# Performance work log

Hardware: AMD Instinct MI355X
Metric: run time of the kernel (lower is better)

## Reference

```python
import jax, jax.numpy as jnp
import numpy as np

HIDDEN = 2048
VOCAB = 50257


def setup_inputs() -> dict:
    key = jax.random.key(0)
    ks = jax.random.split(key, 9)
    s = 1.0 / np.sqrt(HIDDEN)
    return {
        "input": jax.random.randint(ks[0], (1,), 0, VOCAB, dtype=jnp.int64) if jax.config.jax_enable_x64 else jax.random.randint(ks[0], (1,), 0, VOCAB, dtype=jnp.int32),
        "hidden": jax.random.normal(ks[1], (1, 1, HIDDEN), dtype=jnp.float32),
        "embedding": jax.random.normal(ks[2], (VOCAB, HIDDEN), dtype=jnp.float32),
        "w_ih": jax.random.uniform(ks[3], (3 * HIDDEN, HIDDEN), jnp.float32, -s, s),
        "w_hh": jax.random.uniform(ks[4], (3 * HIDDEN, HIDDEN), jnp.float32, -s, s),
        "b_ih": jax.random.uniform(ks[5], (3 * HIDDEN,), jnp.float32, -s, s),
        "b_hh": jax.random.uniform(ks[6], (3 * HIDDEN,), jnp.float32, -s, s),
        "out_w": jax.random.uniform(ks[7], (VOCAB, HIDDEN), jnp.float32, -s, s),
        "out_b": jax.random.uniform(ks[8], (VOCAB,), jnp.float32, -s, s),
    }


def reference(input, hidden, embedding, w_ih, w_hh, b_ih, b_hh, out_w, out_b):
    # embedding lookup + view(1,1,-1) + relu  -> x: [H]
    x = jax.nn.relu(embedding[input[0]])
    h = hidden[0, 0]  # [H]
    # PyTorch GRU single step: gates ordered (r, z, n)
    gi = w_ih @ x + b_ih  # [3H]
    gh = w_hh @ h + b_hh  # [3H]
    i_r, i_z, i_n = jnp.split(gi, 3)
    h_r, h_z, h_n = jnp.split(gh, 3)
    r = jax.nn.sigmoid(i_r + h_r)
    z = jax.nn.sigmoid(i_z + h_z)
    n = jnp.tanh(i_n + r * h_n)
    h_new = (1.0 - z) * n + z * h  # [H]
    # output projection (nn.Linear: x @ W.T + b) + log_softmax(dim=1)
    logits = out_w @ h_new + out_b  # [V]
    logp = jax.nn.log_softmax(logits)[None, :]  # [1, V]
    return logp, h_new[None, None, :]
```

## Files before the change

kernel.cpp:

```cpp
#include <hip/hip_runtime.h>
#include <math.h>

#define H 2048
#define V 50257

__device__ __forceinline__ float wave_reduce_sum(float v) {
#pragma unroll
    for (int off = 32; off > 0; off >>= 1)
        v += __shfl_down(v, off, 64);
    return v;
}

__device__ __forceinline__ float wave_reduce_max(float v) {
#pragma unroll
    for (int off = 32; off > 0; off >>= 1)
        v = fmaxf(v, __shfl_down(v, off, 64));
    return v;
}

__global__ void k_embed(const int* __restrict__ idx_p,
                        const float* __restrict__ emb,
                        float* __restrict__ x) {
    int i = blockIdx.x * blockDim.x + threadIdx.x;
    if (i < H) {
        long idx = (long)idx_p[0];
        float v = emb[idx * (long)H + i];
        x[i] = v > 0.f ? v : 0.f;
    }
}

__global__ __launch_bounds__(384) void k_gru(
    const float* __restrict__ w_ih, const float* __restrict__ w_hh,
    const float* __restrict__ b_ih, const float* __restrict__ b_hh,
    const float* __restrict__ x, const float* __restrict__ hid,
    float* __restrict__ hnew_ws, float* __restrict__ hnew_out) {
    __shared__ float xs[H];
    __shared__ float hs[H];
    __shared__ float partial[6];
    int tid = threadIdx.x;
    for (int i = tid; i < H / 4; i += 384) {
        ((float4*)xs)[i] = ((const float4*)x)[i];
        ((float4*)hs)[i] = ((const float4*)hid)[i];
    }
    __syncthreads();

    int wid = tid >> 6, lane = tid & 63;
    int j = blockIdx.x;
    int gate = wid % 3;
    const float* W = (wid < 3) ? w_ih : w_hh;
    const float* vec = (wid < 3) ? xs : hs;
    const float* row = W + (size_t)(gate * H + j) * (size_t)H;

    float acc = 0.f;
#pragma unroll
    for (int it = 0; it < 8; ++it) {
        float4 w4 = ((const float4*)row)[it * 64 + lane];
        float4 v4 = ((const float4*)vec)[it * 64 + lane];
        acc += w4.x * v4.x + w4.y * v4.y + w4.z * v4.z + w4.w * v4.w;
    }
    acc = wave_reduce_sum(acc);
    if (lane == 0) partial[wid] = acc;
    __syncthreads();

    if (tid == 0) {
        float i_r = partial[0] + b_ih[j];
        float i_z = partial[1] + b_ih[H + j];
        float i_n = partial[2] + b_ih[2 * H + j];
        float h_r = partial[3] + b_hh[j];
        float h_z = partial[4] + b_hh[H + j];
        float h_n = partial[5] + b_hh[2 * H + j];
        float r = 1.f / (1.f + expf(-(i_r + h_r)));
        float z = 1.f / (1.f + expf(-(i_z + h_z)));
        float n = tanhf(i_n + r * h_n);
        float hv = (1.f - z) * n + z * hs[j];
        hnew_ws[j] = hv;
        hnew_out[j] = hv;
    }
}

__global__ __launch_bounds__(256) void k_logits(
    const float* __restrict__ out_w, const float* __restrict__ out_b,
    const float* __restrict__ hnew, float* __restrict__ logits) {
    __shared__ float hs[H];
    int tid = threadIdx.x;
    for (int i = tid; i < H / 4; i += 256)
        ((float4*)hs)[i] = ((const float4*)hnew)[i];
    __syncthreads();

    int wid = tid >> 6, lane = tid & 63;
    int r = blockIdx.x * 4 + wid;
    if (r >= V) return;
    const float* row = out_w + (size_t)r * (size_t)H;

    float acc = 0.f;
#pragma unroll
    for (int it = 0; it < 8; ++it) {
        float4 w4 = ((const float4*)row)[it * 64 + lane];
        float4 v4 = ((const float4*)hs)[it * 64 + lane];
        acc += w4.x * v4.x + w4.y * v4.y + w4.z * v4.z + w4.w * v4.w;
    }
    acc = wave_reduce_sum(acc);
    if (lane == 0) logits[r] = acc + out_b[r];
}

__global__ __launch_bounds__(1024) void k_lse(const float* __restrict__ logits,
                                              float* __restrict__ stats) {
    __shared__ float red[16];
    __shared__ float m_s;
    int tid = threadIdx.x;

    float m = -INFINITY;
    for (int i = tid; i < V; i += 1024) m = fmaxf(m, logits[i]);
    m = wave_reduce_max(m);
    if ((tid & 63) == 0) red[tid >> 6] = m;
    __syncthreads();
    if (tid < 16) {
        m = red[tid];
#pragma unroll
        for (int off = 8; off > 0; off >>= 1)
            m = fmaxf(m, __shfl_down(m, off, 64));
        if (tid == 0) m_s = m;
    }
    __syncthreads();
    float gm = m_s;

    float s = 0.f;
    for (int i = tid; i < V; i += 1024) s += expf(logits[i] - gm);
    s = wave_reduce_sum(s);
    __syncthreads();
    if ((tid & 63) == 0) red[tid >> 6] = s;
    __syncthreads();
    if (tid == 0) {
        float tot = 0.f;
#pragma unroll
        for (int w = 0; w < 16; ++w) tot += red[w];
        stats[0] = gm;
        stats[1] = logf(tot);
    }
}

__global__ void k_finalize(const float* __restrict__ logits,
                           const float* __restrict__ stats,
                           float* __restrict__ out) {
    int i = blockIdx.x * blockDim.x + threadIdx.x;
    if (i < V) out[i] = logits[i] - stats[0] - stats[1];
}

extern "C" void kernel_launch(void* const* d_in, const int* in_sizes, int n_in,
                              void* d_out, int out_size, void* d_ws, size_t ws_size,
                              hipStream_t stream) {
    const int*   idx    = (const int*)d_in[0];
    const float* hidden = (const float*)d_in[1];
    const float* emb    = (const float*)d_in[2];
    const float* w_ih   = (const float*)d_in[3];
    const float* w_hh   = (const float*)d_in[4];
    const float* b_ih   = (const float*)d_in[5];
    const float* b_hh   = (const float*)d_in[6];
    const float* out_w  = (const float*)d_in[7];
    const float* out_b  = (const float*)d_in[8];

    float* out = (float*)d_out;
    float* ws  = (float*)d_ws;
    float* x      = ws;
    float* hnew   = ws + H;
    float* logits = ws + 2 * H;
    float* stats  = ws + 2 * H + ((V + 63) & ~63);

    k_embed<<<(H + 255) / 256, 256, 0, stream>>>(idx, emb, x);
    k_gru<<<H, 384, 0, stream>>>(w_ih, w_hh, b_ih, b_hh, x, hidden, hnew, out + V);
    k_logits<<<(V + 3) / 4, 256, 0, stream>>>(out_w, out_b, hnew, logits);
    k_lse<<<1, 1024, 0, stream>>>(logits, stats);
    k_finalize<<<(V + 255) / 256, 256, 0, stream>>>(logits, stats, out);
}
```

Measured before the change: 117.8 us.

## Fuse embed into GRU, compute online softmax stats in logits kernel

```diff
diff --git a/kernel.cpp b/kernel.cpp
--- a/kernel.cpp
+++ b/kernel.cpp
@@ -3,6 +3,10 @@
 
 #define H 2048
 #define V 50257
+
+#define LOGITS_BLOCKS 2048
+#define LOGITS_WAVES (LOGITS_BLOCKS * 4)
+#define FIN_BLOCKS 52
 
 __device__ __forceinline__ float wave_reduce_sum(float v) {
 #pragma unroll
@@ -11,64 +15,64 @@
     return v;
 }
 
-__device__ __forceinline__ float wave_reduce_max(float v) {
-#pragma unroll
-    for (int off = 32; off > 0; off >>= 1)
-        v = fmaxf(v, __shfl_down(v, off, 64));
-    return v;
-}
-
-__global__ void k_embed(const int* __restrict__ idx_p,
-                        const float* __restrict__ emb,
-                        float* __restrict__ x) {
-    int i = blockIdx.x * blockDim.x + threadIdx.x;
-    if (i < H) {
-        long idx = (long)idx_p[0];
-        float v = emb[idx * (long)H + i];
-        x[i] = v > 0.f ? v : 0.f;
-    }
-}
-
 __global__ __launch_bounds__(384) void k_gru(
+    const int* __restrict__ idx_p,
+    const float* __restrict__ emb,
+    const float* __restrict__ hid,
     const float* __restrict__ w_ih, const float* __restrict__ w_hh,
     const float* __restrict__ b_ih, const float* __restrict__ b_hh,
-    const float* __restrict__ x, const float* __restrict__ hid,
     float* __restrict__ hnew_ws, float* __restrict__ hnew_out) {
     __shared__ float xs[H];
     __shared__ float hs[H];
-    __shared__ float partial[6];
+    __shared__ float partial[6][2];
     int tid = threadIdx.x;
+
+    long idx = (long)idx_p[0];
+    const float4* embrow = (const float4*)(emb + idx * (long)H);
     for (int i = tid; i < H / 4; i += 384) {
-        ((float4*)xs)[i] = ((const float4*)x)[i];
+        float4 e = embrow[i];
+        e.x = fmaxf(e.x, 0.f); e.y = fmaxf(e.y, 0.f);
+        e.z = fmaxf(e.z, 0.f); e.w = fmaxf(e.w, 0.f);
+        ((float4*)xs)[i] = e;
         ((float4*)hs)[i] = ((const float4*)hid)[i];
     }
     __syncthreads();
 
     int wid = tid >> 6, lane = tid & 63;
-    int j = blockIdx.x;
     int gate = wid % 3;
-    const float* W = (wid < 3) ? w_ih : w_hh;
+    const float* W   = (wid < 3) ? w_ih : w_hh;
     const float* vec = (wid < 3) ? xs : hs;
-    const float* row = W + (size_t)(gate * H + j) * (size_t)H;
+    int j0 = blockIdx.x;
+    int j1 = blockIdx.x + 1024;
+    const float4* r0 = (const float4*)(W + ((size_t)gate * H + j0) * (size_t)H);
+    const float4* r1 = (const float4*)(W + ((size_t)gate * H + j1) * (size_t)H);
 
-    float acc = 0.f;
+    float4 vreg[8];
+#pragma unroll
+    for (int it = 0; it < 8; ++it)
+        vreg[it] = ((const float4*)vec)[it * 64 + lane];
+
+    float a0 = 0.f, a1 = 0.f;
 #pragma unroll
     for (int it = 0; it < 8; ++it) {
-        float4 w4 = ((const float4*)row)[it * 64 + lane];
-        float4 v4 = ((const float4*)vec)[it * 64 + lane];
-        acc += w4.x * v4.x + w4.y * v4.y + w4.z * v4.z + w4.w * v4.w;
+        float4 wa = r0[it * 64 + lane];
+        float4 wb = r1[it * 64 + lane];
+        a0 += wa.x * vreg[it].x + wa.y * vreg[it].y + wa.z * vreg[it].z + wa.w * vreg[it].w;
+        a1 += wb.x * vreg[it].x + wb.y * vreg[it].y + wb.z * vreg[it].z + wb.w * vreg[it].w;
     }
-    acc = wave_reduce_sum(acc);
-    if (lane == 0) partial[wid] = acc;
+    a0 = wave_reduce_sum(a0);
+    a1 = wave_reduce_sum(a1);
+    if (lane == 0) { partial[wid][0] = a0; partial[wid][1] = a1; }
     __syncthreads();
 
-    if (tid == 0) {
-        float i_r = partial[0] + b_ih[j];
-        float i_z = partial[1] + b_ih[H + j];
-        float i_n = partial[2] + b_ih[2 * H + j];
-        float h_r = partial[3] + b_hh[j];
-        float h_z = partial[4] + b_hh[H + j];
-        float h_n = partial[5] + b_hh[2 * H + j];
+    if (tid < 2) {
+        int j = (tid == 0) ? j0 : j1;
+        float i_r = partial[0][tid] + b_ih[j];
+        float i_z = partial[1][tid] + b_ih[H + j];
+        float i_n = partial[2][tid] + b_ih[2 * H + j];
+        float h_r = partial[3][tid] + b_hh[j];
+        float h_z = partial[4][tid] + b_hh[H + j];
+        float h_n = partial[5][tid] + b_hh[2 * H + j];
         float r = 1.f / (1.f + expf(-(i_r + h_r)));
         float z = 1.f / (1.f + expf(-(i_z + h_z)));
         float n = tanhf(i_n + r * h_n);
@@ -80,70 +84,93 @@
 
 __global__ __launch_bounds__(256) void k_logits(
     const float* __restrict__ out_w, const float* __restrict__ out_b,
-    const float* __restrict__ hnew, float* __restrict__ logits) {
+    const float* __restrict__ hnew,
+    float* __restrict__ logits, float2* __restrict__ partials) {
     __shared__ float hs[H];
+    __shared__ float pm[4], ps[4];
     int tid = threadIdx.x;
     for (int i = tid; i < H / 4; i += 256)
         ((float4*)hs)[i] = ((const float4*)hnew)[i];
     __syncthreads();
 
     int wid = tid >> 6, lane = tid & 63;
-    int r = blockIdx.x * 4 + wid;
-    if (r >= V) return;
-    const float* row = out_w + (size_t)r * (size_t)H;
+    float4 vreg[8];
+#pragma unroll
+    for (int it = 0; it < 8; ++it)
+        vreg[it] = ((const float4*)hs)[it * 64 + lane];
 
-    float acc = 0.f;
+    float m = -INFINITY, s = 0.f;
+    for (int r = blockIdx.x * 4 + wid; r < V; r += LOGITS_WAVES) {
+        const float4* row = (const float4*)(out_w + (size_t)r * (size_t)H);
+        float acc = 0.f;
 #pragma unroll
-    for (int it = 0; it < 8; ++it) {
-        float4 w4 = ((const float4*)row)[it * 64 + lane];
-        float4 v4 = ((const float4*)hs)[it * 64 + lane];
-        acc += w4.x * v4.x + w4.y * v4.y + w4.z * v4.z + w4.w * v4.w;
+        for (int it = 0; it < 8; ++it) {
+            float4 w4 = row[it * 64 + lane];
+            acc += w4.x * vreg[it].x + w4.y * vreg[it].y + w4.z * vreg[it].z + w4.w * vreg[it].w;
+        }
+        acc = wave_reduce_sum(acc);
+        if (lane == 0) {
+            float l = acc + out_b[r];
+            logits[r] = l;
+            float M = fmaxf(m, l);
+            s = s * __expf(m - M) + __expf(l - M);
+            m = M;
+        }
     }
-    acc = wave_reduce_sum(acc);
-    if (lane == 0) logits[r] = acc + out_b[r];
-}
-
-__global__ __launch_bounds__(1024) void k_lse(const float* __restrict__ logits,
-                                              float* __restrict__ stats) {
-    __shared__ float red[16];
-    __shared__ float m_s;
-    int tid = threadIdx.x;
-
-    float m = -INFINITY;
-    for (int i = tid; i < V; i += 1024) m = fmaxf(m, logits[i]);
-    m = wave_reduce_max(m);
-    if ((tid & 63) == 0) red[tid >> 6] = m;
-    __syncthreads();
-    if (tid < 16) {
-        m = red[tid];
-#pragma unroll
-        for (int off = 8; off > 0; off >>= 1)
-            m = fmaxf(m, __shfl_down(m, off, 64));
-        if (tid == 0) m_s = m;
-    }
-    __syncthreads();
-    float gm = m_s;
-
-    float s = 0.f;
-    for (int i = tid; i < V; i += 1024) s += expf(logits[i] - gm);
-    s = wave_reduce_sum(s);
-    __syncthreads();
-    if ((tid & 63) == 0) red[tid >> 6] = s;
+    if (lane == 0) { pm[wid] = m; ps[wid] = s; }
     __syncthreads();
     if (tid == 0) {
-        float tot = 0.f;
-#pragma unroll
-        for (int w = 0; w < 16; ++w) tot += red[w];
-        stats[0] = gm;
-        stats[1] = logf(tot);
+        float M = fmaxf(fmaxf(pm[0], pm[1]), fmaxf(pm[2], pm[3]));
+        float S = ps[0] * __expf(pm[0] - M) + ps[1] * __expf(pm[1] - M) +
+                  ps[2] * __expf(pm[2] - M) + ps[3] * __expf(pm[3] - M);
+        partials[blockIdx.x] = make_float2(M, S);
     }
 }
 
-__global__ void k_finalize(const float* __restrict__ logits,
-                           const float* __restrict__ stats,
-                           float* __restrict__ out) {
-    int i = blockIdx.x * blockDim.x + threadIdx.x;
-    if (i < V) out[i] = logits[i] - stats[0] - stats[1];
+__global__ __launch_bounds__(256) void k_finalize(
+    const float* __restrict__ logits, const float2* __restrict__ partials,
+    float* __restrict__ out) {
+    __shared__ float pm[4], ps[4];
+    __shared__ float cs;
+    int tid = threadIdx.x;
+
+    float m = -INFINITY, s = 0.f;
+    for (int i = tid; i < LOGITS_BLOCKS; i += 256) {
+        float2 p = partials[i];
+        float M = fmaxf(m, p.x);
+        s = s * __expf(m - M) + p.y * __expf(p.x - M);
+        m = M;
+    }
+#pragma unroll
+    for (int off = 32; off > 0; off >>= 1) {
+        float om = __shfl_down(m, off, 64);
+        float os = __shfl_down(s, off, 64);
+        float M = fmaxf(m, om);
+        s = s * __expf(m - M) + os * __expf(om - M);
+        m = M;
+    }
+    int wid = tid >> 6, lane = tid & 63;
+    if (lane == 0) { pm[wid] = m; ps[wid] = s; }
+    __syncthreads();
+    if (tid == 0) {
+        float M = fmaxf(fmaxf(pm[0], pm[1]), fmaxf(pm[2], pm[3]));
+        float S = ps[0] * __expf(pm[0] - M) + ps[1] * __expf(pm[1] - M) +
+                  ps[2] * __expf(pm[2] - M) + ps[3] * __expf(pm[3] - M);
+        cs = M + logf(S);
+    }
+    __syncthreads();
+    float C = cs;
+
+    int gid = blockIdx.x * 256 + tid;
+    const int nf = V / 4;
+    for (int i = gid; i < nf; i += FIN_BLOCKS * 256) {
+        float4 l4 = ((const float4*)logits)[i];
+        l4.x -= C; l4.y -= C; l4.z -= C; l4.w -= C;
+        ((float4*)out)[i] = l4;
+    }
+    if (gid == 0) {
+        for (int i = nf * 4; i < V; ++i) out[i] = logits[i] - C;
+    }
 }
 
 extern "C" void kernel_launch(void* const* d_in, const int* in_sizes, int n_in,
@@ -161,14 +188,12 @@
 
     float* out = (float*)d_out;
     float* ws  = (float*)d_ws;
-    float* x      = ws;
-    float* hnew   = ws + H;
-    float* logits = ws + 2 * H;
-    float* stats  = ws + 2 * H + ((V + 63) & ~63);
+    float*  hnew     = ws;
+    float*  logits   = ws + H;
+    float2* partials = (float2*)(ws + H + ((V + 1) & ~1));
 
-    k_embed<<<(H + 255) / 256, 256, 0, stream>>>(idx, emb, x);
-    k_gru<<<H, 384, 0, stream>>>(w_ih, w_hh, b_ih, b_hh, x, hidden, hnew, out + V);
-    k_logits<<<(V + 3) / 4, 256, 0, stream>>>(out_w, out_b, hnew, logits);
-    k_lse<<<1, 1024, 0, stream>>>(logits, stats);
-    k_finalize<<<(V + 255) / 256, 256, 0, stream>>>(logits, stats, out);
+    k_gru<<<1024, 384, 0, stream>>>(idx, emb, hidden, w_ih, w_hh, b_ih, b_hh,
+                                    hnew, out + V);
+    k_logits<<<LOGITS_BLOCKS, 256, 0, stream>>>(out_w, out_b, hnew, logits, partials);
+    k_finalize<<<FIN_BLOCKS, 256, 0, stream>>>(logits, partials, out);
 }
```

Measured after the change: 100.0 us. 15.1% less time.
